# Performance work log

Measured on AMD Instinct MI355X. Metric: run time of the kernel, lower is better.

The kernel has to match this reference:

```python
import jax, jax.numpy as jnp
import numpy as np
from jax import lax

B, T, H = 32768, 64, 16
VOCAB_USER = 600001
VOCAB_LAUNCH = 3


def setup_inputs() -> dict:
    key = jax.random.key(0)
    ks = jax.random.split(key, 10)
    s = 1.0 / np.sqrt(H)
    return {
        "user_id": jax.random.randint(ks[0], (B,), 0, VOCAB_USER),
        "launch_seq": jax.random.randint(ks[1], (B, T), 0, VOCAB_LAUNCH),
        "user_emb": jax.random.normal(ks[2], (VOCAB_USER, H), dtype=jnp.float32),
        "launch_emb": jax.random.normal(ks[3], (VOCAB_LAUNCH, H), dtype=jnp.float32),
        "W_ih": jax.random.uniform(ks[4], (3 * H, H), jnp.float32, -s, s),
        "W_hh": jax.random.uniform(ks[5], (3 * H, H), jnp.float32, -s, s),
        "b_ih": jax.random.uniform(ks[6], (3 * H,), jnp.float32, -s, s),
        "b_hh": jax.random.uniform(ks[7], (3 * H,), jnp.float32, -s, s),
        "fc_W": jax.random.uniform(ks[8], (1, 2 * H), jnp.float32, -s, s),
        "fc_b": jax.random.uniform(ks[9], (1,), jnp.float32, -s, s),
    }


def reference(user_id, launch_seq, user_emb, launch_emb, W_ih, W_hh, b_ih, b_hh, fc_W, fc_b):
    u = user_emb[user_id]                      # (B, H)
    x = launch_emb[launch_seq]                 # (B, T, H)
    # precompute input contributions to the gates for all timesteps
    gx_all = jnp.einsum('bth,gh->btg', x, W_ih) + b_ih  # (B, T, 3H)

    def step(h, gx):
        gh = h @ W_hh.T + b_hh                 # (B, 3H)
        r = jax.nn.sigmoid(gx[:, :H] + gh[:, :H])
        z = jax.nn.sigmoid(gx[:, H:2 * H] + gh[:, H:2 * H])
        n = jnp.tanh(gx[:, 2 * H:] + r * gh[:, 2 * H:])
        h_new = (1.0 - z) * n + z * h
        return h_new, h_new

    h0 = jnp.zeros((x.shape[0], H), dtype=x.dtype)
    _, hs = lax.scan(step, h0, jnp.swapaxes(gx_all, 0, 1))  # hs: (T, B, H)
    pooled = jnp.mean(hs, axis=0)              # (B, H)
    fc_in = jnp.concatenate([u, pooled], axis=1)  # (B, 2H)
    return fc_in @ fc_W.T + fc_b               # (B, 1)
```

## Files before the change

kernel.cpp:

```cpp
#include <hip/hip_runtime.h>
#include <hip/hip_bf16.h>
#include <string.h>


#define NBLK 2048

typedef __attribute__((ext_vector_type(8))) short   short8;
typedef __attribute__((ext_vector_type(4))) float   floatx4;
typedef __attribute__((ext_vector_type(4))) unsigned uintx4;

static __device__ __forceinline__ float fexp2(float x) { return __builtin_amdgcn_exp2f(x); }
static __device__ __forceinline__ float frcp(float x)  { return __builtin_amdgcn_rcpf(x); }
static __device__ __forceinline__ unsigned f2u(float f) { unsigned u; memcpy(&u, &f, 4); return u; }
static __device__ __forceinline__ float u2f(unsigned u) { float f; memcpy(&f, &u, 4); return f; }
static __device__ __forceinline__ unsigned short bf16_rne(float f) {
    union { __hip_bfloat16 b; unsigned short u; } cv; cv.b = __float2bfloat16(f); return cv.u;
}
static __device__ __forceinline__ float sel3(int c, float a0, float a1, float a2) {
    return c == 0 ? a0 : (c == 1 ? a1 : a2);
}

__global__ __launch_bounds__(64) void gru_mfma(
    const int* __restrict__ user_id,
    const int* __restrict__ launch_seq,
    const float* __restrict__ user_emb,
    const float* __restrict__ launch_emb,
    const float* __restrict__ W_ih,
    const float* __restrict__ W_hh,
    const float* __restrict__ b_ih,
    const float* __restrict__ b_hh,
    const float* __restrict__ fc_W,
    const float* __restrict__ fc_b,
    float* __restrict__ out)
{
    constexpr float L  = 1.4426950408889634f;
    constexpr float L2 = 2.8853900817779268f;

    __shared__ float         gxlut[192];
    __shared__ unsigned char seqT[1024];
    __shared__ unsigned      hlds[512];

    const int tid  = threadIdx.x;
    const int col  = tid & 15;
    const int quad = tid >> 4;
    const long long sampBase = (long long)blockIdx.x * 16;

    {
        int r = tid >> 2, w = tid & 3;
        const int* sp = launch_seq + (sampBase + r) * 64 + w * 16;
        #pragma unroll
        for (int g = 0; g < 4; ++g) {
            int4 v = ((const int4*)sp)[g];
            int t0 = w * 16 + g * 4;
            seqT[(t0 + 0) * 16 + r] = (unsigned char)v.x;
            seqT[(t0 + 1) * 16 + r] = (unsigned char)v.y;
            seqT[(t0 + 2) * 16 + r] = (unsigned char)v.z;
            seqT[(t0 + 3) * 16 + r] = (unsigned char)v.w;
        }
    }

    for (int idx = tid; idx < 144; idx += 64) {
        int s = idx / 48, g = idx - s * 48;
        float dot = b_ih[g];
        #pragma unroll
        for (int k = 0; k < 16; ++k)
            dot = fmaf(W_ih[g * 16 + k], launch_emb[s * 16 + k], dot);
        gxlut[g * 4 + s] = (g < 32) ? (-L * (dot + b_hh[g])) : (L2 * dot);
    }

    short8 Brh, Brl, Bzh, Bzl, Bnh, Bnl;
    #pragma unroll
    for (int j = 0; j < 8; ++j) {
        int k = quad * 8 + j;
        float wr = 0.f, wz = 0.f, wn = 0.f;
        if (k < 16) {
            wr = -L  * W_hh[(col)      * 16 + k];
            wz = -L  * W_hh[(16 + col) * 16 + k];
            wn =  L2 * W_hh[(32 + col) * 16 + k];
        }
        unsigned short hb;
        hb = bf16_rne(wr); Brh[j] = (short)hb; Brl[j] = (short)bf16_rne(wr - u2f((unsigned)hb << 16));
        hb = bf16_rne(wz); Bzh[j] = (short)hb; Bzl[j] = (short)bf16_rne(wz - u2f((unsigned)hb << 16));
        hb = bf16_rne(wn); Bnh[j] = (short)hb; Bnl[j] = (short)bf16_rne(wn - u2f((unsigned)hb << 16));
    }
    const float bhn = L2 * b_hh[32 + col];
    const floatx4 CnInit = {bhn, bhn, bhn, bhn};

    __syncthreads();

    float4 vr = *(const float4*)&gxlut[(col)      * 4];
    float4 vz = *(const float4*)&gxlut[(16 + col) * 4];
    float4 vn = *(const float4*)&gxlut[(32 + col) * 4];

    const int qa = quad & 1;
    const int p0 = ((qa * 8) + 4 * ((col >> 1) & 3)) & 15;
    const int a_dw1 = col * 16 + p0;
    const int a_dw2 = col * 16 + ((p0 + 4) & 15);
    int w_dw[4];
    #pragma unroll
    for (int i = 0; i < 4; ++i) {
        int s = quad * 4 + i;
        w_dw[i] = s * 16 + ((col + 4 * ((s >> 1) & 3)) & 15);
    }

    floatx4 h    = {0.f, 0.f, 0.f, 0.f};
    floatx4 pool = {0.f, 0.f, 0.f, 0.f};
    short8 Ahi = {0, 0, 0, 0, 0, 0, 0, 0};
    short8 Alo = {0, 0, 0, 0, 0, 0, 0, 0};
    unsigned seq_dw = *(const unsigned*)&seqT[quad * 4];

    #pragma unroll 4
    for (int t = 0; t < 64; ++t) {
        const int wb = (t & 1) ? 256 : 0;

        int c0 = seq_dw & 3, c1 = (seq_dw >> 8) & 3,
            c2 = (seq_dw >> 16) & 3, c3 = (seq_dw >> 24) & 3;
        floatx4 accr = { sel3(c0, vr.x, vr.y, vr.z), sel3(c1, vr.x, vr.y, vr.z),
                         sel3(c2, vr.x, vr.y, vr.z), sel3(c3, vr.x, vr.y, vr.z) };
        floatx4 accz = { sel3(c0, vz.x, vz.y, vz.z), sel3(c1, vz.x, vz.y, vz.z),
                         sel3(c2, vz.x, vz.y, vz.z), sel3(c3, vz.x, vz.y, vz.z) };
        float gn[4]  = { sel3(c0, vn.x, vn.y, vn.z), sel3(c1, vn.x, vn.y, vn.z),
                         sel3(c2, vn.x, vn.y, vn.z), sel3(c3, vn.x, vn.y, vn.z) };

        seq_dw = *(const unsigned*)&seqT[((t + 1) & 63) * 16 + quad * 4];

        accr = __builtin_amdgcn_mfma_f32_16x16x32_bf16(Ahi, Brh, accr, 0, 0, 0);
        accz = __builtin_amdgcn_mfma_f32_16x16x32_bf16(Ahi, Bzh, accz, 0, 0, 0);
        floatx4 accn = __builtin_amdgcn_mfma_f32_16x16x32_bf16(Ahi, Bnh, CnInit, 0, 0, 0);
        accr = __builtin_amdgcn_mfma_f32_16x16x32_bf16(Alo, Brh, accr, 0, 0, 0);
        accz = __builtin_amdgcn_mfma_f32_16x16x32_bf16(Alo, Bzh, accz, 0, 0, 0);
        accn = __builtin_amdgcn_mfma_f32_16x16x32_bf16(Alo, Bnh, accn, 0, 0, 0);
        accr = __builtin_amdgcn_mfma_f32_16x16x32_bf16(Ahi, Brl, accr, 0, 0, 0);
        accz = __builtin_amdgcn_mfma_f32_16x16x32_bf16(Ahi, Bzl, accz, 0, 0, 0);
        accn = __builtin_amdgcn_mfma_f32_16x16x32_bf16(Ahi, Bnl, accn, 0, 0, 0);

        #pragma unroll
        for (int i = 0; i < 4; ++i) {
            float r  = frcp(1.0f + fexp2(accr[i]));
            float z  = frcp(1.0f + fexp2(accz[i]));
            float y  = fmaf(r, accn[i], gn[i]);
            float n  = fmaf(-2.0f, frcp(1.0f + fexp2(y)), 1.0f);
            float hn = fmaf(z, h[i] - n, n);
            h[i] = hn;
            pool[i] += hn;
            unsigned u  = f2u(hn);
            float  lof  = hn - u2f(u & 0xffff0000u);
            hlds[wb + w_dw[i]] = __builtin_amdgcn_perm(f2u(lof), u, 0x07060302u);
        }

        uintx4 A1 = *(const uintx4*)&hlds[wb + a_dw1];
        uintx4 A2 = *(const uintx4*)&hlds[wb + a_dw2];
        uintx4 hi4 = { __builtin_amdgcn_perm(A1.y, A1.x, 0x05040100u),
                       __builtin_amdgcn_perm(A1.w, A1.z, 0x05040100u),
                       __builtin_amdgcn_perm(A2.y, A2.x, 0x05040100u),
                       __builtin_amdgcn_perm(A2.w, A2.z, 0x05040100u) };
        uintx4 lo4 = { __builtin_amdgcn_perm(A1.y, A1.x, 0x07060302u),
                       __builtin_amdgcn_perm(A1.w, A1.z, 0x07060302u),
                       __builtin_amdgcn_perm(A2.y, A2.x, 0x07060302u),
                       __builtin_amdgcn_perm(A2.w, A2.z, 0x07060302u) };
        Ahi = __builtin_bit_cast(short8, hi4);
        Alo = __builtin_bit_cast(short8, lo4);
    }

    const float fw1 = fc_W[col];
    const float fw2 = fc_W[16 + col] * (1.0f / 64.0f);
    #pragma unroll
    for (int i = 0; i < 4; ++i) {
        int s = quad * 4 + i;
        int uid = user_id[sampBase + s];
        float u = user_emb[(long long)uid * 16 + col];
        float v = fmaf(u, fw1, pool[i] * fw2);
        v += __shfl_xor(v, 1);
        v += __shfl_xor(v, 2);
        v += __shfl_xor(v, 4);
        v += __shfl_xor(v, 8);
        if (col == 0) out[sampBase + s] = v + fc_b[0];
    }
}

extern "C" void kernel_launch(void* const* d_in, const int* in_sizes, int n_in,
                              void* d_out, int out_size, void* d_ws, size_t ws_size,
                              hipStream_t stream) {
    const int*   user_id    = (const int*)d_in[0];
    const int*   launch_seq = (const int*)d_in[1];
    const float* user_emb   = (const float*)d_in[2];
    const float* launch_emb = (const float*)d_in[3];
    const float* W_ih       = (const float*)d_in[4];
    const float* W_hh       = (const float*)d_in[5];
    const float* b_ih       = (const float*)d_in[6];
    const float* b_hh       = (const float*)d_in[7];
    const float* fc_W       = (const float*)d_in[8];
    const float* fc_b       = (const float*)d_in[9];
    float* out = (float*)d_out;

    gru_mfma<<<dim3(NBLK), dim3(64), 0, stream>>>(
        user_id, launch_seq, user_emb, launch_emb,
        W_ih, W_hh, b_ih, b_hh, fc_W, fc_b, out);
}
```

Before: 145.1 us.

## Transpose GRU MFMA so hidden state feeds back via ds_bpermute instead of LDS

```diff
diff --git a/kernel.cpp b/kernel.cpp
--- a/kernel.cpp
+++ b/kernel.cpp
@@ -5,17 +5,14 @@
 
 #define NBLK 2048
 
-typedef __attribute__((ext_vector_type(8))) short   short8;
-typedef __attribute__((ext_vector_type(4))) float   floatx4;
+typedef __attribute__((ext_vector_type(8))) short    short8;
+typedef __attribute__((ext_vector_type(4))) float    floatx4;
 typedef __attribute__((ext_vector_type(4))) unsigned uintx4;
 
 static __device__ __forceinline__ float fexp2(float x) { return __builtin_amdgcn_exp2f(x); }
 static __device__ __forceinline__ float frcp(float x)  { return __builtin_amdgcn_rcpf(x); }
 static __device__ __forceinline__ unsigned f2u(float f) { unsigned u; memcpy(&u, &f, 4); return u; }
 static __device__ __forceinline__ float u2f(unsigned u) { float f; memcpy(&f, &u, 4); return f; }
-static __device__ __forceinline__ unsigned short bf16_rne(float f) {
-    union { __hip_bfloat16 b; unsigned short u; } cv; cv.b = __float2bfloat16(f); return cv.u;
-}
 static __device__ __forceinline__ float sel3(int c, float a0, float a1, float a2) {
     return c == 0 ? a0 : (c == 1 ? a1 : a2);
 }
@@ -36,9 +33,8 @@
     constexpr float L  = 1.4426950408889634f;
     constexpr float L2 = 2.8853900817779268f;
 
-    __shared__ float         gxlut[192];
+    __shared__ float         gxlut[144];
     __shared__ unsigned char seqT[1024];
-    __shared__ unsigned      hlds[512];
 
     const int tid  = threadIdx.x;
     const int col  = tid & 15;
@@ -65,117 +61,138 @@
         #pragma unroll
         for (int k = 0; k < 16; ++k)
             dot = fmaf(W_ih[g * 16 + k], launch_emb[s * 16 + k], dot);
-        gxlut[g * 4 + s] = (g < 32) ? (-L * (dot + b_hh[g])) : (L2 * dot);
-    }
-
-    short8 Brh, Brl, Bzh, Bzl, Bnh, Bnl;
-    #pragma unroll
-    for (int j = 0; j < 8; ++j) {
-        int k = quad * 8 + j;
-        float wr = 0.f, wz = 0.f, wn = 0.f;
-        if (k < 16) {
-            wr = -L  * W_hh[(col)      * 16 + k];
-            wz = -L  * W_hh[(16 + col) * 16 + k];
-            wn =  L2 * W_hh[(32 + col) * 16 + k];
-        }
-        unsigned short hb;
-        hb = bf16_rne(wr); Brh[j] = (short)hb; Brl[j] = (short)bf16_rne(wr - u2f((unsigned)hb << 16));
-        hb = bf16_rne(wz); Bzh[j] = (short)hb; Bzl[j] = (short)bf16_rne(wz - u2f((unsigned)hb << 16));
-        hb = bf16_rne(wn); Bnh[j] = (short)hb; Bnl[j] = (short)bf16_rne(wn - u2f((unsigned)hb << 16));
-    }
-    const float bhn = L2 * b_hh[32 + col];
-    const floatx4 CnInit = {bhn, bhn, bhn, bhn};
+        int gate = g >> 4, dim = g & 15;
+        gxlut[(gate * 3 + s) * 16 + dim] =
+            (g < 32) ? (-L * (dot + b_hh[g])) : (L2 * dot);
+    }
+
+    short8 Wrh, Wrl, Wzh, Wzl, Wnh, Wnl;
+    {
+        auto makeW = [&](int goff, float scale, short8& Hi, short8& Lo) {
+            float w[8];
+            if (quad < 2) {
+                const float* row = W_hh + (goff + col) * 16 + quad * 8;
+                float4 a = *(const float4*)row;
+                float4 b = *(const float4*)(row + 4);
+                w[0] = scale * a.x; w[1] = scale * a.y; w[2] = scale * a.z; w[3] = scale * a.w;
+                w[4] = scale * b.x; w[5] = scale * b.y; w[6] = scale * b.z; w[7] = scale * b.w;
+            } else {
+                #pragma unroll
+                for (int j = 0; j < 8; ++j) w[j] = 0.f;
+            }
+            uintx4 hi, lo;
+            #pragma unroll
+            for (int p = 0; p < 4; ++p) {
+                unsigned u0 = f2u(w[2 * p]), u1 = f2u(w[2 * p + 1]);
+                hi[p] = __builtin_amdgcn_perm(u1, u0, 0x07060302u);
+                float l0 = w[2 * p]     - u2f(u0 & 0xffff0000u);
+                float l1 = w[2 * p + 1] - u2f(u1 & 0xffff0000u);
+                lo[p] = __builtin_amdgcn_perm(f2u(l1), f2u(l0), 0x07060302u);
+            }
+            Hi = __builtin_bit_cast(short8, hi);
+            Lo = __builtin_bit_cast(short8, lo);
+        };
+        makeW(0,  -L, Wrh, Wrl);
+        makeW(16, -L, Wzh, Wzl);
+        makeW(32,  L2, Wnh, Wnl);
+    }
+
+    floatx4 CnInit;
+    {
+        float4 bh = *(const float4*)&b_hh[32 + quad * 4];
+        CnInit = floatx4{L2 * bh.x, L2 * bh.y, L2 * bh.z, L2 * bh.w};
+    }
 
     __syncthreads();
 
-    float4 vr = *(const float4*)&gxlut[(col)      * 4];
-    float4 vz = *(const float4*)&gxlut[(16 + col) * 4];
-    float4 vn = *(const float4*)&gxlut[(32 + col) * 4];
-
-    const int qa = quad & 1;
-    const int p0 = ((qa * 8) + 4 * ((col >> 1) & 3)) & 15;
-    const int a_dw1 = col * 16 + p0;
-    const int a_dw2 = col * 16 + ((p0 + 4) & 15);
-    int w_dw[4];
-    #pragma unroll
-    for (int i = 0; i < 4; ++i) {
-        int s = quad * 4 + i;
-        w_dw[i] = s * 16 + ((col + 4 * ((s >> 1) & 3)) & 15);
-    }
+    floatx4 gr0 = *(const floatx4*)&gxlut[(0 * 3 + 0) * 16 + quad * 4];
+    floatx4 gr1 = *(const floatx4*)&gxlut[(0 * 3 + 1) * 16 + quad * 4];
+    floatx4 gr2 = *(const floatx4*)&gxlut[(0 * 3 + 2) * 16 + quad * 4];
+    floatx4 gz0 = *(const floatx4*)&gxlut[(1 * 3 + 0) * 16 + quad * 4];
+    floatx4 gz1 = *(const floatx4*)&gxlut[(1 * 3 + 1) * 16 + quad * 4];
+    floatx4 gz2 = *(const floatx4*)&gxlut[(1 * 3 + 2) * 16 + quad * 4];
+    floatx4 gn0 = *(const floatx4*)&gxlut[(2 * 3 + 0) * 16 + quad * 4];
+    floatx4 gn1 = *(const floatx4*)&gxlut[(2 * 3 + 1) * 16 + quad * 4];
+    floatx4 gn2 = *(const floatx4*)&gxlut[(2 * 3 + 2) * 16 + quad * 4];
+
+    const int a1 = (col + 32 * (quad & 1)) * 4;
+    const int a2 = a1 + 64;
 
     floatx4 h    = {0.f, 0.f, 0.f, 0.f};
     floatx4 pool = {0.f, 0.f, 0.f, 0.f};
-    short8 Ahi = {0, 0, 0, 0, 0, 0, 0, 0};
-    short8 Alo = {0, 0, 0, 0, 0, 0, 0, 0};
-    unsigned seq_dw = *(const unsigned*)&seqT[quad * 4];
+    short8 Bhi = {0, 0, 0, 0, 0, 0, 0, 0};
+    short8 Blo = {0, 0, 0, 0, 0, 0, 0, 0};
+    int c = seqT[col];
 
     #pragma unroll 4
     for (int t = 0; t < 64; ++t) {
-        const int wb = (t & 1) ? 256 : 0;
-
-        int c0 = seq_dw & 3, c1 = (seq_dw >> 8) & 3,
-            c2 = (seq_dw >> 16) & 3, c3 = (seq_dw >> 24) & 3;
-        floatx4 accr = { sel3(c0, vr.x, vr.y, vr.z), sel3(c1, vr.x, vr.y, vr.z),
-                         sel3(c2, vr.x, vr.y, vr.z), sel3(c3, vr.x, vr.y, vr.z) };
-        floatx4 accz = { sel3(c0, vz.x, vz.y, vz.z), sel3(c1, vz.x, vz.y, vz.z),
-                         sel3(c2, vz.x, vz.y, vz.z), sel3(c3, vz.x, vz.y, vz.z) };
-        float gn[4]  = { sel3(c0, vn.x, vn.y, vn.z), sel3(c1, vn.x, vn.y, vn.z),
-                         sel3(c2, vn.x, vn.y, vn.z), sel3(c3, vn.x, vn.y, vn.z) };
-
-        seq_dw = *(const unsigned*)&seqT[((t + 1) & 63) * 16 + quad * 4];
-
-        accr = __builtin_amdgcn_mfma_f32_16x16x32_bf16(Ahi, Brh, accr, 0, 0, 0);
-        accz = __builtin_amdgcn_mfma_f32_16x16x32_bf16(Ahi, Bzh, accz, 0, 0, 0);
-        floatx4 accn = __builtin_amdgcn_mfma_f32_16x16x32_bf16(Ahi, Bnh, CnInit, 0, 0, 0);
-        accr = __builtin_amdgcn_mfma_f32_16x16x32_bf16(Alo, Brh, accr, 0, 0, 0);
-        accz = __builtin_amdgcn_mfma_f32_16x16x32_bf16(Alo, Bzh, accz, 0, 0, 0);
-        accn = __builtin_amdgcn_mfma_f32_16x16x32_bf16(Alo, Bnh, accn, 0, 0, 0);
-        accr = __builtin_amdgcn_mfma_f32_16x16x32_bf16(Ahi, Brl, accr, 0, 0, 0);
-        accz = __builtin_amdgcn_mfma_f32_16x16x32_bf16(Ahi, Bzl, accz, 0, 0, 0);
-        accn = __builtin_amdgcn_mfma_f32_16x16x32_bf16(Ahi, Bnl, accn, 0, 0, 0);
+        floatx4 accr, accz, gnv;
+        #pragma unroll
+        for (int i = 0; i < 4; ++i) {
+            accr[i] = sel3(c, gr0[i], gr1[i], gr2[i]);
+            accz[i] = sel3(c, gz0[i], gz1[i], gz2[i]);
+            gnv[i]  = sel3(c, gn0[i], gn1[i], gn2[i]);
+        }
+        int cn = seqT[((t + 1) & 63) * 16 + col];
+
+        accr = __builtin_amdgcn_mfma_f32_16x16x32_bf16(Wrh, Bhi, accr, 0, 0, 0);
+        accz = __builtin_amdgcn_mfma_f32_16x16x32_bf16(Wzh, Bhi, accz, 0, 0, 0);
+        floatx4 accn = __builtin_amdgcn_mfma_f32_16x16x32_bf16(Wnh, Bhi, CnInit, 0, 0, 0);
+        accr = __builtin_amdgcn_mfma_f32_16x16x32_bf16(Wrl, Bhi, accr, 0, 0, 0);
+        accz = __builtin_amdgcn_mfma_f32_16x16x32_bf16(Wzl, Bhi, accz, 0, 0, 0);
+        accn = __builtin_amdgcn_mfma_f32_16x16x32_bf16(Wnl, Bhi, accn, 0, 0, 0);
+        accr = __builtin_amdgcn_mfma_f32_16x16x32_bf16(Wrh, Blo, accr, 0, 0, 0);
+        accz = __builtin_amdgcn_mfma_f32_16x16x32_bf16(Wzh, Blo, accz, 0, 0, 0);
+        accn = __builtin_amdgcn_mfma_f32_16x16x32_bf16(Wnh, Blo, accn, 0, 0, 0);
 
         #pragma unroll
         for (int i = 0; i < 4; ++i) {
             float r  = frcp(1.0f + fexp2(accr[i]));
             float z  = frcp(1.0f + fexp2(accz[i]));
-            float y  = fmaf(r, accn[i], gn[i]);
+            float y  = fmaf(r, accn[i], gnv[i]);
             float n  = fmaf(-2.0f, frcp(1.0f + fexp2(y)), 1.0f);
             float hn = fmaf(z, h[i] - n, n);
             h[i] = hn;
             pool[i] += hn;
-            unsigned u  = f2u(hn);
-            float  lof  = hn - u2f(u & 0xffff0000u);
-            hlds[wb + w_dw[i]] = __builtin_amdgcn_perm(f2u(lof), u, 0x07060302u);
         }
 
-        uintx4 A1 = *(const uintx4*)&hlds[wb + a_dw1];
-        uintx4 A2 = *(const uintx4*)&hlds[wb + a_dw2];
-        uintx4 hi4 = { __builtin_amdgcn_perm(A1.y, A1.x, 0x05040100u),
-                       __builtin_amdgcn_perm(A1.w, A1.z, 0x05040100u),
-                       __builtin_amdgcn_perm(A2.y, A2.x, 0x05040100u),
-                       __builtin_amdgcn_perm(A2.w, A2.z, 0x05040100u) };
-        uintx4 lo4 = { __builtin_amdgcn_perm(A1.y, A1.x, 0x07060302u),
-                       __builtin_amdgcn_perm(A1.w, A1.z, 0x07060302u),
-                       __builtin_amdgcn_perm(A2.y, A2.x, 0x07060302u),
-                       __builtin_amdgcn_perm(A2.w, A2.z, 0x07060302u) };
-        Ahi = __builtin_bit_cast(short8, hi4);
-        Alo = __builtin_bit_cast(short8, lo4);
-    }
-
-    const float fw1 = fc_W[col];
-    const float fw2 = fc_W[16 + col] * (1.0f / 64.0f);
-    #pragma unroll
-    for (int i = 0; i < 4; ++i) {
-        int s = quad * 4 + i;
-        int uid = user_id[sampBase + s];
-        float u = user_emb[(long long)uid * 16 + col];
-        float v = fmaf(u, fw1, pool[i] * fw2);
-        v += __shfl_xor(v, 1);
-        v += __shfl_xor(v, 2);
-        v += __shfl_xor(v, 4);
-        v += __shfl_xor(v, 8);
-        if (col == 0) out[sampBase + s] = v + fc_b[0];
-    }
+        unsigned u0 = f2u(h[0]), u1 = f2u(h[1]), u2 = f2u(h[2]), u3 = f2u(h[3]);
+        unsigned hp0 = __builtin_amdgcn_perm(u1, u0, 0x07060302u);
+        unsigned hp1 = __builtin_amdgcn_perm(u3, u2, 0x07060302u);
+        float l0 = h[0] - u2f(u0 & 0xffff0000u);
+        float l1 = h[1] - u2f(u1 & 0xffff0000u);
+        float l2 = h[2] - u2f(u2 & 0xffff0000u);
+        float l3 = h[3] - u2f(u3 & 0xffff0000u);
+        unsigned lp0 = __builtin_amdgcn_perm(f2u(l1), f2u(l0), 0x07060302u);
+        unsigned lp1 = __builtin_amdgcn_perm(f2u(l3), f2u(l2), 0x07060302u);
+
+        uintx4 bh4, bl4;
+        bh4[0] = (unsigned)__builtin_amdgcn_ds_bpermute(a1, (int)hp0);
+        bh4[1] = (unsigned)__builtin_amdgcn_ds_bpermute(a1, (int)hp1);
+        bh4[2] = (unsigned)__builtin_amdgcn_ds_bpermute(a2, (int)hp0);
+        bh4[3] = (unsigned)__builtin_amdgcn_ds_bpermute(a2, (int)hp1);
+        bl4[0] = (unsigned)__builtin_amdgcn_ds_bpermute(a1, (int)lp0);
+        bl4[1] = (unsigned)__builtin_amdgcn_ds_bpermute(a1, (int)lp1);
+        bl4[2] = (unsigned)__builtin_amdgcn_ds_bpermute(a2, (int)lp0);
+        bl4[3] = (unsigned)__builtin_amdgcn_ds_bpermute(a2, (int)lp1);
+        Bhi = __builtin_bit_cast(short8, bh4);
+        Blo = __builtin_bit_cast(short8, bl4);
+        c = cn;
+    }
+
+    float4 fc1 = *(const float4*)&fc_W[quad * 4];
+    float4 fc2 = *(const float4*)&fc_W[16 + quad * 4];
+    int uid = user_id[sampBase + col];
+    float4 u4 = *(const float4*)&user_emb[(long long)uid * 16 + quad * 4];
+    const float inv64 = 1.0f / 64.0f;
+    float val = fc1.x * u4.x + fc1.y * u4.y + fc1.z * u4.z + fc1.w * u4.w;
+    val = fmaf(fc2.x * inv64, pool[0], val);
+    val = fmaf(fc2.y * inv64, pool[1], val);
+    val = fmaf(fc2.z * inv64, pool[2], val);
+    val = fmaf(fc2.w * inv64, pool[3], val);
+    val += __shfl_xor(val, 16);
+    val += __shfl_xor(val, 32);
+    if (quad == 0) out[sampBase + col] = val + fc_b[0];
 }
 
 extern "C" void kernel_launch(void* const* d_in, const int* in_sizes, int n_in,
```

Result: faster. 138.1 us (-4.8%).
